# Optimization experiments

Hardware: AMD Instinct MI355X
Metric: run time of the kernel (lower is better)

## Reference

```python
import jax, jax.numpy as jnp
import numpy as np

# Static config matching AdaConv(c_in=512, p=4, batch_size=8, s_d=512, c_out=512)
C_IN = 512
C_OUT = 512
N_GROUPS = 128  # c_in // p


def _conv(x, w, b, groups=1, padding='VALID'):
    # x: NCHW, w: OIHW
    y = jax.lax.conv_general_dilated(
        x, w, window_strides=(1, 1), padding=padding,
        dimension_numbers=('NCHW', 'OIHW', 'NCHW'),
        feature_group_count=groups)
    return y + b[None, :, None, None]


def setup_inputs() -> dict:
    key = jax.random.key(0)
    ks = jax.random.split(key, 9)
    f32 = jnp.float32
    s = 0.02  # small init scale to keep activations well-behaved
    inp = {
        'style_encoding': jax.random.normal(ks[0], (8, 512, 4, 4), f32),
        'predicted': jax.random.normal(ks[1], (8, 512, 64, 64), f32),
        'dw1_w': jax.random.normal(ks[2], (512, 512, 1, 1), f32) * s,
        'dw1_b': jnp.full((512,), 0.01, f32),
        'dw2_w': jax.random.normal(ks[3], (2048, 512, 2, 2), f32) * s,
        'dw2_b': jnp.full((2048,), 0.01, f32),
        'pk1_w': jax.random.normal(ks[4], (512, 512, 1, 1), f32) * s,
        'pk1_b': jnp.full((512,), 0.01, f32),
        'pk2_w': jax.random.normal(ks[5], (2048, 512, 1, 1), f32) * s,
        'pk2_b': jnp.full((2048,), 0.01, f32),
        'pb1_w': jax.random.normal(ks[6], (512, 512, 1, 1), f32) * s,
        'pb1_b': jnp.full((512,), 0.01, f32),
        'pb2_w': jax.random.normal(ks[7], (512, 512, 1, 1), f32) * s,
        'pb2_b': jnp.full((512,), 0.01, f32),
    }
    return inp


def reference(style_encoding, predicted,
              dw1_w, dw1_b, dw2_w, dw2_b,
              pk1_w, pk1_b, pk2_w, pk2_b,
              pb1_w, pb1_b, pb2_w, pb2_b):
    N = style_encoding.shape[0]
    lrelu = lambda x: jax.nn.leaky_relu(x, 0.01)

    # --- predict per-sample depthwise 3x3 kernels from style (4x4 -> 3x3) ---
    h = lrelu(_conv(style_encoding, dw1_w, dw1_b))           # [N, c_in, 4, 4]
    depthwise = _conv(h, dw2_w, dw2_b)                       # [N, c_out*(c_in/n_groups), 3, 3]
    depthwise = depthwise.reshape(N * C_OUT, C_IN // N_GROUPS, 3, 3)

    # --- predict per-sample pointwise kernels + bias from pooled style ---
    s_pool = jnp.mean(style_encoding, axis=(2, 3), keepdims=True)  # [N, s_d, 1, 1]
    pk = _conv(lrelu(_conv(s_pool, pk1_w, pk1_b)), pk2_w, pk2_b)
    pointwise_kn = pk.reshape(N * C_OUT, C_OUT // N_GROUPS, 1, 1)
    pb = _conv(lrelu(_conv(s_pool, pb1_w, pb1_b)), pb2_w, pb2_b)
    pointwise_bias = pb.reshape(N * C_OUT)

    # --- apply per-sample dynamic conv via huge-group grouped conv trick ---
    a, b, c, d = predicted.shape
    x = predicted.reshape(1, a * b, c, d)
    x = jnp.pad(x, ((0, 0), (0, 0), (1, 1), (1, 1)), mode='reflect')
    batch_groups = N * N_GROUPS
    y = jax.lax.conv_general_dilated(
        x, depthwise, (1, 1), 'VALID',
        dimension_numbers=('NCHW', 'OIHW', 'NCHW'),
        feature_group_count=batch_groups)                    # [1, N*c_out, c, d]
    y = jax.lax.conv_general_dilated(
        y, pointwise_kn, (1, 1), 'VALID',
        dimension_numbers=('NCHW', 'OIHW', 'NCHW'),
        feature_group_count=batch_groups)
    y = y + pointwise_bias[None, :, None, None]
    # permute([1,0,2,3]).view(a,b,c,d) with leading dim 1 == plain reshape
    return y.reshape(a, b, c, d)
```

## Files before the change

### kernel.cpp

```cpp
#include <hip/hip_runtime.h>

#define LRELU(x) ((x) > 0.f ? (x) : 0.01f * (x))

#define H2_OFF    0
#define T1_OFF    65536
#define T2_OFF    69632
#define PK_OFF    73728
#define PB_OFF    90112
#define WB_OFF    241664

__global__ __launch_bounds__(256) void kA(const float* __restrict__ style,
    const float* __restrict__ dw1_w, const float* __restrict__ dw1_b,
    const float* __restrict__ pk1_w, const float* __restrict__ pk1_b,
    const float* __restrict__ pb1_w, const float* __restrict__ pb1_b,
    float* __restrict__ h2t, float* __restrict__ t1, float* __restrict__ t2) {
  int b = blockIdx.x;
  int tid = threadIdx.x;
  __shared__ float smem[512];
  int wave = tid >> 6, l = tid & 63;
  float sv[8];
  const float* w;
  const float* bv;
  int cobase;
  if (b < 512) {
    int n = b >> 6; int pix = (b >> 2) & 15; int cq = b & 3;
    const float* sp = style + n * 8192 + pix;
#pragma unroll
    for (int j = 0; j < 8; ++j) sv[j] = sp[(8 * l + j) * 16];
    w = dw1_w; bv = dw1_b;
    cobase = cq * 128 + wave * 32;
    float res = (l < 32) ? bv[cobase + l] : 0.f;
#pragma unroll 8
    for (int j = 0; j < 32; ++j) {
      const float4* wr = (const float4*)(w + (cobase + j) * 512 + 8 * l);
      float4 a = wr[0], c = wr[1];
      float v = a.x*sv[0] + a.y*sv[1] + a.z*sv[2] + a.w*sv[3]
              + c.x*sv[4] + c.y*sv[5] + c.z*sv[6] + c.w*sv[7];
      v += __shfl_xor(v, 1);
      v += __shfl_xor(v, 2);
      v += __shfl_xor(v, 4);
      v += __shfl_xor(v, 8);
      v += __shfl_xor(v, 16);
      v += __shfl_xor(v, 32);
      if (l == j) res += v;
    }
    if (l < 32) h2t[n * 8192 + (cobase + l) * 16 + pix] = LRELU(res);
  } else {
    int b2 = b - 512;
    int cq = b2 & 3; int which = (b2 >> 2) & 1; int n = b2 >> 3;
    for (int ci = tid; ci < 512; ci += 256) {
      const float4* r4 = (const float4*)(style + n * 8192 + ci * 16);
      float4 a = r4[0], bb = r4[1], c = r4[2], d = r4[3];
      smem[ci] = (a.x+a.y+a.z+a.w + bb.x+bb.y+bb.z+bb.w + c.x+c.y+c.z+c.w + d.x+d.y+d.z+d.w) * (1.f/16.f);
    }
    __syncthreads();
#pragma unroll
    for (int j = 0; j < 8; ++j) sv[j] = smem[8 * l + j];
    w  = which ? pb1_w : pk1_w;
    bv = which ? pb1_b : pk1_b;
    cobase = cq * 128 + wave * 32;
    float* outp = (which ? t2 : t1) + n * 512;
    float res = (l < 32) ? bv[cobase + l] : 0.f;
#pragma unroll 8
    for (int j = 0; j < 32; ++j) {
      const float4* wr = (const float4*)(w + (cobase + j) * 512 + 8 * l);
      float4 a = wr[0], c = wr[1];
      float v = a.x*sv[0] + a.y*sv[1] + a.z*sv[2] + a.w*sv[3]
              + c.x*sv[4] + c.y*sv[5] + c.z*sv[6] + c.w*sv[7];
      v += __shfl_xor(v, 1);
      v += __shfl_xor(v, 2);
      v += __shfl_xor(v, 4);
      v += __shfl_xor(v, 8);
      v += __shfl_xor(v, 16);
      v += __shfl_xor(v, 32);
      if (l == j) res += v;
    }
    if (l < 32) outp[cobase + l] = LRELU(res);
  }
}

__global__ __launch_bounds__(256) void kB(const float* __restrict__ h2t,
    const float* __restrict__ dw2_w,
    const float* __restrict__ t1, const float* __restrict__ t2,
    const float* __restrict__ pk2_w, const float* __restrict__ pk2_b,
    const float* __restrict__ pb2_w, const float* __restrict__ pb2_b,
    float* __restrict__ PART, float* __restrict__ pk, float* __restrict__ pb) {
  __shared__ float smem[6784];
  int b = blockIdx.x;
  int tid = threadIdx.x;
  if (b < 512) {
    int kc = b & 15; int bo = (b >> 4) & 15; int nh = b >> 8;
    float* Wt = smem;
    float* ht = smem + 4224;
    {
      int run = tid >> 1; int half = tid & 1;
      int nn = run >> 5; int ci = run & 31;
      const float* src = h2t + (nh * 4 + nn) * 8192 + (kc * 32 + ci) * 16 + half * 8;
      float4 v0 = *(const float4*)src;
      float4 v1 = *(const float4*)(src + 4);
      float* dst = &ht[run * 20 + half * 8];
      *(float4*)dst = v0;
      *(float4*)(dst + 4) = v1;
    }
    int lane = tid & 127; int nng = tid >> 7;
    float acc[2][9];
#pragma unroll
    for (int nn = 0; nn < 2; ++nn)
#pragma unroll
      for (int p = 0; p < 9; ++p) acc[nn][p] = 0.f;
#pragma unroll 1
    for (int sc = 0; sc < 4; ++sc) {
      __syncthreads();
#pragma unroll
      for (int m = 0; m < 4; ++m) {
        int row = m * 32 + (tid >> 3); int kc4 = tid & 7;
        float4 v = *(const float4*)(dw2_w + (size_t)(bo * 128 + row) * 2048 + kc * 128 + sc * 32 + kc4 * 4);
        Wt[(kc4 * 4 + 0) * 132 + row] = v.x;
        Wt[(kc4 * 4 + 1) * 132 + row] = v.y;
        Wt[(kc4 * 4 + 2) * 132 + row] = v.z;
        Wt[(kc4 * 4 + 3) * 132 + row] = v.w;
      }
      __syncthreads();
#pragma unroll
      for (int cil = 0; cil < 8; ++cil) {
        int ci = sc * 8 + cil;
        float wx = Wt[(cil * 4 + 0) * 132 + lane];
        float wy = Wt[(cil * 4 + 1) * 132 + lane];
        float wz = Wt[(cil * 4 + 2) * 132 + lane];
        float ww = Wt[(cil * 4 + 3) * 132 + lane];
#pragma unroll
        for (int nn = 0; nn < 2; ++nn) {
          const float* hrow = &ht[((nng * 2 + nn) * 32 + ci) * 20];
          float4 a0 = *(const float4*)(hrow + 0);
          float4 a1 = *(const float4*)(hrow + 4);
          float4 a2 = *(const float4*)(hrow + 8);
          float4 a3 = *(const float4*)(hrow + 12);
          float vv[16];
          vv[0]=a0.x; vv[1]=a0.y; vv[2]=a0.z; vv[3]=a0.w;
          vv[4]=a1.x; vv[5]=a1.y; vv[6]=a1.z; vv[7]=a1.w;
          vv[8]=a2.x; vv[9]=a2.y; vv[10]=a2.z; vv[11]=a2.w;
          vv[12]=a3.x; vv[13]=a3.y; vv[14]=a3.z; vv[15]=a3.w;
#pragma unroll
          for (int p = 0; p < 9; ++p) {
            int r = (p / 3) * 4 + (p % 3);
            acc[nn][p] += wx * vv[r] + wy * vv[r + 1] + wz * vv[r + 4] + ww * vv[r + 5];
          }
        }
      }
    }
#pragma unroll
    for (int nn = 0; nn < 2; ++nn) {
      int n = nh * 4 + nng * 2 + nn;
#pragma unroll
      for (int p = 0; p < 9; ++p)
        PART[(size_t)kc * 147456 + ((n * 9 + p) * 2048) + bo * 128 + lane] = acc[nn][p];
    }
  } else {
    int b2 = b - 512;
    int n = b2 / 20; int t20 = b2 % 20;
    bool isPb = t20 >= 16;
    int cobase = (isPb ? (t20 - 16) : t20) * 128;
    float* s = smem;
    const float* src = (isPb ? t2 : t1) + n * 512;
    for (int i = tid; i < 512; i += 256) s[i] = src[i];
    __syncthreads();
    int wave = tid >> 6, l = tid & 63;
    float sv[8];
#pragma unroll
    for (int j = 0; j < 8; ++j) sv[j] = s[8 * l + j];
    const float* w  = isPb ? pb2_w : pk2_w;
    const float* bv = isPb ? pb2_b : pk2_b;
    int cg = cobase + wave * 32;
    float res = (l < 32) ? bv[cg + l] : 0.f;
#pragma unroll 8
    for (int j = 0; j < 32; ++j) {
      const float4* wr = (const float4*)(w + (cg + j) * 512 + 8 * l);
      float4 a = wr[0], c = wr[1];
      float v = a.x*sv[0] + a.y*sv[1] + a.z*sv[2] + a.w*sv[3]
              + c.x*sv[4] + c.y*sv[5] + c.z*sv[6] + c.w*sv[7];
      v += __shfl_xor(v, 1);
      v += __shfl_xor(v, 2);
      v += __shfl_xor(v, 4);
      v += __shfl_xor(v, 8);
      v += __shfl_xor(v, 16);
      v += __shfl_xor(v, 32);
      if (l == j) res += v;
    }
    if (l < 32) {
      if (isPb) pb[n * 512 + cg + l] = res;
      else      pk[n * 2048 + cg + l] = res;
    }
  }
}

__global__ __launch_bounds__(256) void kW(const float* __restrict__ PART,
    const float* __restrict__ pk, const float* __restrict__ dw2_b,
    const float* __restrict__ pb, float* __restrict__ wbuf) {
  int idx = blockIdx.x * 256 + threadIdx.x;
  if (idx >= 8 * 128 * 160) return;
  int t = idx % 160; int Qn = idx / 160; int Q = Qn & 127; int n = Qn >> 7;
  if (t >= 144) {
    wbuf[idx] = (t < 148) ? pb[n * 512 + Q * 4 + (t - 144)] : 0.f;
    return;
  }
  int o = t & 3; int u = t >> 2; int kx = u % 3; int v = u / 3;
  int i = v & 3; int ky = v >> 2; int p = ky * 3 + kx;
  const float* pkp = pk + n * 2048 + 16 * Q + 4 * o;
  const float* bp  = dw2_b + 16 * Q;
  size_t dbase = (size_t)(n * 9 + p) * 2048 + 16 * Q;
  float sum = 0.f;
#pragma unroll
  for (int j = 0; j < 4; ++j) {
    float dv = bp[4 * j + i];
    size_t off = dbase + 4 * j + i;
#pragma unroll
    for (int s = 0; s < 16; ++s) dv += PART[(size_t)s * 147456 + off];
    sum += pkp[j] * dv;
  }
  wbuf[idx] = sum;
}

__global__ __launch_bounds__(256) void kC(const float* __restrict__ x,
    const float* __restrict__ wbuf, float* __restrict__ out) {
  int b = blockIdx.x; int rt = b & 3; int Q = (b >> 2) & 127; int n = b >> 9;
  const float* wb = wbuf + (size_t)(n * 128 + Q) * 160;
  const float* base = x + (size_t)(n * 512 + Q * 4) * 4096;
  int e = threadIdx.x & 15;
  int y = rt * 16 + (threadIdx.x >> 4);
  int x0 = 4 * e;
  int ro[3];
#pragma unroll
  for (int ky = 0; ky < 3; ++ky) {
    int ry = y - 1 + ky;
    ry = ry < 0 ? 1 : (ry > 63 ? 62 : ry);
    ro[ky] = ry * 64;
  }
  float acc[4][4];
#pragma unroll
  for (int o = 0; o < 4; ++o) {
    float bv = wb[144 + o];
#pragma unroll
    for (int px = 0; px < 4; ++px) acc[o][px] = bv;
  }
#pragma unroll
  for (int i = 0; i < 4; ++i) {
    const float* ci = base + i * 4096;
#pragma unroll
    for (int ky = 0; ky < 3; ++ky) {
      float4 v0 = *(const float4*)(ci + ro[ky] + x0);
      float vl = __shfl_up(v0.w, 1, 16);
      float vr = __shfl_down(v0.x, 1, 16);
      if (e == 0)  vl = v0.y;
      if (e == 15) vr = v0.z;
      float va0 = vl, va1 = v0.x, va2 = v0.y, va3 = v0.z, va4 = v0.w, va5 = vr;
#pragma unroll
      for (int kx = 0; kx < 3; ++kx) {
        const float* wp = &wb[((ky * 4 + i) * 3 + kx) * 4];
        float w0 = wp[0], w1 = wp[1], w2 = wp[2], w3 = wp[3];
        float xv0 = kx == 0 ? va0 : (kx == 1 ? va1 : va2);
        float xv1 = kx == 0 ? va1 : (kx == 1 ? va2 : va3);
        float xv2 = kx == 0 ? va2 : (kx == 1 ? va3 : va4);
        float xv3 = kx == 0 ? va3 : (kx == 1 ? va4 : va5);
        acc[0][0] += w0 * xv0; acc[0][1] += w0 * xv1; acc[0][2] += w0 * xv2; acc[0][3] += w0 * xv3;
        acc[1][0] += w1 * xv0; acc[1][1] += w1 * xv1; acc[1][2] += w1 * xv2; acc[1][3] += w1 * xv3;
        acc[2][0] += w2 * xv0; acc[2][1] += w2 * xv1; acc[2][2] += w2 * xv2; acc[2][3] += w2 * xv3;
        acc[3][0] += w3 * xv0; acc[3][1] += w3 * xv1; acc[3][2] += w3 * xv2; acc[3][3] += w3 * xv3;
      }
    }
  }
#pragma unroll
  for (int o = 0; o < 4; ++o) {
    float4 st; st.x = acc[o][0]; st.y = acc[o][1]; st.z = acc[o][2]; st.w = acc[o][3];
    *(float4*)&out[(((size_t)(n * 512 + Q * 4 + o)) * 64 + y) * 64 + x0] = st;
  }
}

extern "C" void kernel_launch(void* const* d_in, const int* in_sizes, int n_in,
                              void* d_out, int out_size, void* d_ws, size_t ws_size,
                              hipStream_t stream) {
  const float* style = (const float*)d_in[0];
  const float* pred  = (const float*)d_in[1];
  const float* dw1_w = (const float*)d_in[2];
  const float* dw1_b = (const float*)d_in[3];
  const float* dw2_w = (const float*)d_in[4];
  const float* dw2_b = (const float*)d_in[5];
  const float* pk1_w = (const float*)d_in[6];
  const float* pk1_b = (const float*)d_in[7];
  const float* pk2_w = (const float*)d_in[8];
  const float* pk2_b = (const float*)d_in[9];
  const float* pb1_w = (const float*)d_in[10];
  const float* pb1_b = (const float*)d_in[11];
  const float* pb2_w = (const float*)d_in[12];
  const float* pb2_b = (const float*)d_in[13];
  float* ws  = (float*)d_ws;
  float* h2t = ws + H2_OFF;
  float* t1  = ws + T1_OFF;
  float* t2  = ws + T2_OFF;
  float* pk  = ws + PK_OFF;
  float* pb  = ws + PB_OFF;
  float* wb  = ws + WB_OFF;
  float* out = (float*)d_out;
  float* PART = out;

  kA<<<576, 256, 0, stream>>>(style, dw1_w, dw1_b, pk1_w, pk1_b, pb1_w, pb1_b, h2t, t1, t2);
  kB<<<672, 256, 0, stream>>>(h2t, dw2_w, t1, t2, pk2_w, pk2_b, pb2_w, pb2_b, PART, pk, pb);
  kW<<<640, 256, 0, stream>>>(PART, pk, dw2_b, pb, wb);
  kC<<<4096, 256, 0, stream>>>(pred, wb, out);
}
```

Measured before the change: 71.42 us.

## Split dw2 reduction over more blocks and prefetch next channel rows in kC

The dw2 GEMM in kB now splits the K dimension into 32 chunks instead of 16 and handles 2 samples per block instead of 4, which quadruples the block count so more CUs stay busy. kW now sums 32 partial slices instead of 16. In kC, the three input rows for the next channel are loaded before the current channel's FMAs run, to hide global load latency. The cost is twice the partial-sum traffic and reduction work, and higher register pressure in kC.

```diff
diff --git a/kernel.cpp b/kernel.cpp
--- a/kernel.cpp
+++ b/kernel.cpp
@@ -19,20 +19,16 @@
   __shared__ float smem[512];
   int wave = tid >> 6, l = tid & 63;
   float sv[8];
-  const float* w;
-  const float* bv;
-  int cobase;
   if (b < 512) {
     int n = b >> 6; int pix = (b >> 2) & 15; int cq = b & 3;
     const float* sp = style + n * 8192 + pix;
 #pragma unroll
     for (int j = 0; j < 8; ++j) sv[j] = sp[(8 * l + j) * 16];
-    w = dw1_w; bv = dw1_b;
-    cobase = cq * 128 + wave * 32;
-    float res = (l < 32) ? bv[cobase + l] : 0.f;
+    int cobase = cq * 128 + wave * 32;
+    float res = (l < 32) ? dw1_b[cobase + l] : 0.f;
 #pragma unroll 8
     for (int j = 0; j < 32; ++j) {
-      const float4* wr = (const float4*)(w + (cobase + j) * 512 + 8 * l);
+      const float4* wr = (const float4*)(dw1_w + (cobase + j) * 512 + 8 * l);
       float4 a = wr[0], c = wr[1];
       float v = a.x*sv[0] + a.y*sv[1] + a.z*sv[2] + a.w*sv[3]
               + c.x*sv[4] + c.y*sv[5] + c.z*sv[6] + c.w*sv[7];
@@ -56,9 +52,9 @@
     __syncthreads();
 #pragma unroll
     for (int j = 0; j < 8; ++j) sv[j] = smem[8 * l + j];
-    w  = which ? pb1_w : pk1_w;
-    bv = which ? pb1_b : pk1_b;
-    cobase = cq * 128 + wave * 32;
+    const float* w  = which ? pb1_w : pk1_w;
+    const float* bv = which ? pb1_b : pk1_b;
+    int cobase = cq * 128 + wave * 32;
     float* outp = (which ? t2 : t1) + n * 512;
     float res = (l < 32) ? bv[cobase + l] : 0.f;
 #pragma unroll 8
@@ -85,36 +81,32 @@
     const float* __restrict__ pk2_w, const float* __restrict__ pk2_b,
     const float* __restrict__ pb2_w, const float* __restrict__ pb2_b,
     float* __restrict__ PART, float* __restrict__ pk, float* __restrict__ pb) {
-  __shared__ float smem[6784];
+  __shared__ float smem[4864];
   int b = blockIdx.x;
   int tid = threadIdx.x;
-  if (b < 512) {
-    int kc = b & 15; int bo = (b >> 4) & 15; int nh = b >> 8;
+  if (b < 2048) {
+    int kc = b & 31; int bo = (b >> 5) & 15; int ng = b >> 9;
     float* Wt = smem;
     float* ht = smem + 4224;
-    {
-      int run = tid >> 1; int half = tid & 1;
-      int nn = run >> 5; int ci = run & 31;
-      const float* src = h2t + (nh * 4 + nn) * 8192 + (kc * 32 + ci) * 16 + half * 8;
-      float4 v0 = *(const float4*)src;
-      float4 v1 = *(const float4*)(src + 4);
-      float* dst = &ht[run * 20 + half * 8];
-      *(float4*)dst = v0;
-      *(float4*)(dst + 4) = v1;
+    if (tid < 128) {
+      int run = tid >> 2; int q = tid & 3;
+      int nn = run >> 4; int cil = run & 15;
+      const float* src = h2t + (size_t)(ng * 2 + nn) * 8192 + (kc * 16 + cil) * 16 + q * 4;
+      float4 v = *(const float4*)src;
+      *(float4*)&ht[run * 20 + q * 4] = v;
     }
     int lane = tid & 127; int nng = tid >> 7;
-    float acc[2][9];
-#pragma unroll
-    for (int nn = 0; nn < 2; ++nn)
-#pragma unroll
-      for (int p = 0; p < 9; ++p) acc[nn][p] = 0.f;
+    int n = ng * 2 + nng;
+    float acc[9];
+#pragma unroll
+    for (int p = 0; p < 9; ++p) acc[p] = 0.f;
 #pragma unroll 1
-    for (int sc = 0; sc < 4; ++sc) {
+    for (int sc = 0; sc < 2; ++sc) {
       __syncthreads();
 #pragma unroll
       for (int m = 0; m < 4; ++m) {
         int row = m * 32 + (tid >> 3); int kc4 = tid & 7;
-        float4 v = *(const float4*)(dw2_w + (size_t)(bo * 128 + row) * 2048 + kc * 128 + sc * 32 + kc4 * 4);
+        float4 v = *(const float4*)(dw2_w + (size_t)(bo * 128 + row) * 2048 + kc * 64 + sc * 32 + kc4 * 4);
         Wt[(kc4 * 4 + 0) * 132 + row] = v.x;
         Wt[(kc4 * 4 + 1) * 132 + row] = v.y;
         Wt[(kc4 * 4 + 2) * 132 + row] = v.z;
@@ -123,40 +115,32 @@
       __syncthreads();
 #pragma unroll
       for (int cil = 0; cil < 8; ++cil) {
-        int ci = sc * 8 + cil;
         float wx = Wt[(cil * 4 + 0) * 132 + lane];
         float wy = Wt[(cil * 4 + 1) * 132 + lane];
         float wz = Wt[(cil * 4 + 2) * 132 + lane];
         float ww = Wt[(cil * 4 + 3) * 132 + lane];
-#pragma unroll
-        for (int nn = 0; nn < 2; ++nn) {
-          const float* hrow = &ht[((nng * 2 + nn) * 32 + ci) * 20];
-          float4 a0 = *(const float4*)(hrow + 0);
-          float4 a1 = *(const float4*)(hrow + 4);
-          float4 a2 = *(const float4*)(hrow + 8);
-          float4 a3 = *(const float4*)(hrow + 12);
-          float vv[16];
-          vv[0]=a0.x; vv[1]=a0.y; vv[2]=a0.z; vv[3]=a0.w;
-          vv[4]=a1.x; vv[5]=a1.y; vv[6]=a1.z; vv[7]=a1.w;
-          vv[8]=a2.x; vv[9]=a2.y; vv[10]=a2.z; vv[11]=a2.w;
-          vv[12]=a3.x; vv[13]=a3.y; vv[14]=a3.z; vv[15]=a3.w;
-#pragma unroll
-          for (int p = 0; p < 9; ++p) {
-            int r = (p / 3) * 4 + (p % 3);
-            acc[nn][p] += wx * vv[r] + wy * vv[r + 1] + wz * vv[r + 4] + ww * vv[r + 5];
-          }
+        const float* hrow = &ht[(nng * 16 + sc * 8 + cil) * 20];
+        float4 a0 = *(const float4*)(hrow + 0);
+        float4 a1 = *(const float4*)(hrow + 4);
+        float4 a2 = *(const float4*)(hrow + 8);
+        float4 a3 = *(const float4*)(hrow + 12);
+        float vv[16];
+        vv[0]=a0.x; vv[1]=a0.y; vv[2]=a0.z; vv[3]=a0.w;
+        vv[4]=a1.x; vv[5]=a1.y; vv[6]=a1.z; vv[7]=a1.w;
+        vv[8]=a2.x; vv[9]=a2.y; vv[10]=a2.z; vv[11]=a2.w;
+        vv[12]=a3.x; vv[13]=a3.y; vv[14]=a3.z; vv[15]=a3.w;
+#pragma unroll
+        for (int p = 0; p < 9; ++p) {
+          int r = (p / 3) * 4 + (p % 3);
+          acc[p] += wx * vv[r] + wy * vv[r + 1] + wz * vv[r + 4] + ww * vv[r + 5];
         }
       }
     }
 #pragma unroll
-    for (int nn = 0; nn < 2; ++nn) {
-      int n = nh * 4 + nng * 2 + nn;
-#pragma unroll
-      for (int p = 0; p < 9; ++p)
-        PART[(size_t)kc * 147456 + ((n * 9 + p) * 2048) + bo * 128 + lane] = acc[nn][p];
-    }
+    for (int p = 0; p < 9; ++p)
+      PART[(size_t)kc * 147456 + ((n * 9 + p) * 2048) + bo * 128 + lane] = acc[p];
   } else {
-    int b2 = b - 512;
+    int b2 = b - 2048;
     int n = b2 / 20; int t20 = b2 % 20;
     bool isPb = t20 >= 16;
     int cobase = (isPb ? (t20 - 16) : t20) * 128;
@@ -214,7 +198,7 @@
     float dv = bp[4 * j + i];
     size_t off = dbase + 4 * j + i;
 #pragma unroll
-    for (int s = 0; s < 16; ++s) dv += PART[(size_t)s * 147456 + off];
+    for (int s = 0; s < 32; ++s) dv += PART[(size_t)s * 147456 + off];
     sum += pkp[j] * dv;
   }
   wbuf[idx] = sum;
@@ -242,17 +226,29 @@
 #pragma unroll
     for (int px = 0; px < 4; ++px) acc[o][px] = bv;
   }
+  float4 cur[3];
+#pragma unroll
+  for (int ky = 0; ky < 3; ++ky) cur[ky] = *(const float4*)(base + ro[ky] + x0);
 #pragma unroll
   for (int i = 0; i < 4; ++i) {
-    const float* ci = base + i * 4096;
+    float4 nxt[3];
+    if (i < 3) {
+#pragma unroll
+      for (int ky = 0; ky < 3; ++ky)
+        nxt[ky] = *(const float4*)(base + (i + 1) * 4096 + ro[ky] + x0);
+    }
+    float vl[3], vr[3];
 #pragma unroll
     for (int ky = 0; ky < 3; ++ky) {
-      float4 v0 = *(const float4*)(ci + ro[ky] + x0);
-      float vl = __shfl_up(v0.w, 1, 16);
-      float vr = __shfl_down(v0.x, 1, 16);
-      if (e == 0)  vl = v0.y;
-      if (e == 15) vr = v0.z;
-      float va0 = vl, va1 = v0.x, va2 = v0.y, va3 = v0.z, va4 = v0.w, va5 = vr;
+      vl[ky] = __shfl_up(cur[ky].w, 1, 16);
+      vr[ky] = __shfl_down(cur[ky].x, 1, 16);
+      if (e == 0)  vl[ky] = cur[ky].y;
+      if (e == 15) vr[ky] = cur[ky].z;
+    }
+#pragma unroll
+    for (int ky = 0; ky < 3; ++ky) {
+      float va0 = vl[ky], va1 = cur[ky].x, va2 = cur[ky].y, va3 = cur[ky].z,
+            va4 = cur[ky].w, va5 = vr[ky];
 #pragma unroll
       for (int kx = 0; kx < 3; ++kx) {
         const float* wp = &wb[((ky * 4 + i) * 3 + kx) * 4];
@@ -266,6 +262,10 @@
         acc[2][0] += w2 * xv0; acc[2][1] += w2 * xv1; acc[2][2] += w2 * xv2; acc[2][3] += w2 * xv3;
         acc[3][0] += w3 * xv0; acc[3][1] += w3 * xv1; acc[3][2] += w3 * xv2; acc[3][3] += w3 * xv3;
       }
+    }
+    if (i < 3) {
+#pragma unroll
+      for (int ky = 0; ky < 3; ++ky) cur[ky] = nxt[ky];
     }
   }
 #pragma unroll
@@ -303,7 +303,7 @@
   float* PART = out;
 
   kA<<<576, 256, 0, stream>>>(style, dw1_w, dw1_b, pk1_w, pk1_b, pb1_w, pb1_b, h2t, t1, t2);
-  kB<<<672, 256, 0, stream>>>(h2t, dw2_w, t1, t2, pk2_w, pk2_b, pb2_w, pb2_b, PART, pk, pb);
+  kB<<<2208, 256, 0, stream>>>(h2t, dw2_w, t1, t2, pk2_w, pk2_b, pb2_w, pb2_b, PART, pk, pb);
   kW<<<640, 256, 0, stream>>>(PART, pk, dw2_b, pb, wb);
   kC<<<4096, 256, 0, stream>>>(pred, wb, out);
 }
```

After: 98.20 us. 1.38x slower.
